# Kernel tuning notes

Hardware: AMD Instinct MI355X
Metric: run time of the kernel (lower is better)

Reference implementation:

```python
import jax, jax.numpy as jnp
import numpy as np
from jax import lax

BETA = 0.3

def setup_inputs() -> dict:
    key = jax.random.key(0)
    ks = jax.random.split(key, 5)
    B, C, H, W = 1, 64, 96, 96
    x = jax.random.normal(ks[0], (B, C, H, W), dtype=jnp.float32)
    # d_conv: Conv2d(C, C, k=3, stride=1, padding=2, dilation=2)
    dW = jax.random.normal(ks[1], (C, C, 3, 3), dtype=jnp.float32) * 0.05
    db = jax.random.normal(ks[2], (C,), dtype=jnp.float32) * 0.05
    # conv: Conv2d(C, C, k=1)
    cW = jax.random.normal(ks[3], (C, C, 1, 1), dtype=jnp.float32) * 0.1
    cb = jax.random.normal(ks[4], (C,), dtype=jnp.float32) * 0.05
    return {"x": x, "dW": dW, "db": db, "cW": cW, "cb": cb}

def _conv(x, w, b, padding, dilation):
    y = lax.conv_general_dilated(
        x, w, window_strides=(1, 1),
        padding=[(padding, padding), (padding, padding)],
        rhs_dilation=(dilation, dilation),
        dimension_numbers=("NCHW", "OIHW", "NCHW"))
    return y + b[None, :, None, None]

def reference(x, dW, db, cW, cb):
    B, C, H, W = x.shape
    HW = H * W
    y = _conv(x, dW, db, padding=2, dilation=2)   # (B,C,H,W), same d_conv used for q and k
    v = _conv(x, cW, cb, padding=0, dilation=1).reshape(B, HW, C)
    # NOTE: torch uses raw .reshape (not transpose) for q — faithful here.
    q = y.reshape(B, HW, C)
    k = y.reshape(B, C, HW)
    qk = jnp.einsum("bnc,bcm->bnm", q, k)         # (B,HW,HW)
    qk = jnp.where(jnp.abs(qk) > BETA, qk, 0.0)   # threshold mask (qk*mask)
    att = jax.nn.softmax(qk, axis=-1)
    att = jnp.einsum("bnm,bmc->bnc", att, v)      # (B,HW,C)
    att = att.swapaxes(1, 2).reshape(B, C, H, W)
    return x + att
```

## Files before the change

kernel.cpp:

```cpp
#include <hip/hip_runtime.h>
#include <hip/hip_bf16.h>

#define CC 64
#define HW 9216
#define IMG 96
#define SPLITS 8
#define SPLEN 1152
#define ITERS 18
#define LOG2E 1.44269504f

typedef _Float16 f16;
typedef __attribute__((ext_vector_type(8))) _Float16 f16x8;
typedef __attribute__((ext_vector_type(4))) _Float16 f16x4;
typedef __attribute__((ext_vector_type(2))) _Float16 f16x2;
typedef __attribute__((ext_vector_type(4))) float f32x4;

__global__ __launch_bounds__(256) void prepad_kernel(
    const float* __restrict__ x, f16* __restrict__ xt)
{
    __shared__ float tile[64][65];
    const int p0 = blockIdx.x * 64;
    const int t = threadIdx.x;
    const int pl = t & 63;
    const int p = p0 + pl;
    int r = p / 100, c = p % 100;
    bool interior = (r >= 2) && (r < 98) && (c >= 2) && (c < 98);
    int img = (r - 2) * IMG + (c - 2);
    #pragma unroll
    for (int j = 0; j < 16; ++j) {
        int ci = j * 4 + (t >> 6);
        tile[pl][ci] = interior ? x[ci * HW + img] : 0.f;
    }
    __syncthreads();
    const int row16 = t >> 4, chunk = t & 15;
    #pragma unroll
    for (int j = 0; j < 4; ++j) {
        int row = j * 16 + row16;
        int pr = p0 + row;
        if (pr < 10000) {
            f16x4 hv = {(f16)tile[row][chunk * 4 + 0], (f16)tile[row][chunk * 4 + 1],
                        (f16)tile[row][chunk * 4 + 2], (f16)tile[row][chunk * 4 + 3]};
            *(f16x4*)&xt[pr * 64 + chunk * 4] = hv;
        }
    }
}

__global__ __launch_bounds__(256) void conv_mfma_kernel(
    const f16* __restrict__ xt, const float* __restrict__ dW, const float* __restrict__ db,
    const float* __restrict__ cW, const float* __restrict__ cb,
    f16* __restrict__ yq, f16* __restrict__ kt, f16* __restrict__ vt)
{
    __shared__ f16 Wl[9 * 16 * 64];
    __shared__ f16 cWl[16 * 64];

    const int b = blockIdx.x;
    const int mblk = b >> 2, cog = b & 3;
    const int co0 = cog * 16;
    const int t = threadIdx.x;

    #pragma unroll 4
    for (int j = 0; j < 36; ++j) {
        int d = j * 256 + t;
        int tap = d >> 10, rem = d & 1023, co = rem >> 6, ci = rem & 63;
        Wl[d] = (f16)dW[(co0 + co) * 576 + ci * 9 + tap];
    }
    #pragma unroll
    for (int j = 0; j < 4; ++j) {
        int d = j * 256 + t;
        cWl[d] = (f16)cW[(co0 + (d >> 6)) * CC + (d & 63)];
    }
    __syncthreads();

    const int w = t >> 6, L = t & 63, g = L >> 4, c16 = L & 15;
    const int ms = mblk * 64 + w * 16;
    const int h = ms / IMG, wc = ms % IMG;
    const int pb = (h + 2) * 100 + (wc + 2) + c16;

    f16x8 Bf[9][2], Bv[2];
    #pragma unroll
    for (int tap = 0; tap < 9; ++tap)
        #pragma unroll
        for (int kc = 0; kc < 2; ++kc)
            Bf[tap][kc] = *(const f16x8*)&Wl[(tap * 16 + c16) * 64 + g * 8 + kc * 32];
    #pragma unroll
    for (int kc = 0; kc < 2; ++kc)
        Bv[kc] = *(const f16x8*)&cWl[c16 * 64 + g * 8 + kc * 32];

    f32x4 accY = (f32x4){0.f, 0.f, 0.f, 0.f};
    f32x4 accV = (f32x4){0.f, 0.f, 0.f, 0.f};

    #pragma unroll
    for (int tap = 0; tap < 9; ++tap) {
        int kh = tap / 3, kw = tap % 3;
        int toff = (2 * kh - 2) * 100 + (2 * kw - 2);
        const f16* ap = xt + (pb + toff) * 64;
        f16x8 A0 = *(const f16x8*)(ap + g * 8);
        f16x8 A1 = *(const f16x8*)(ap + g * 8 + 32);
        accY = __builtin_amdgcn_mfma_f32_16x16x32_f16(A0, Bf[tap][0], accY, 0, 0, 0);
        accY = __builtin_amdgcn_mfma_f32_16x16x32_f16(A1, Bf[tap][1], accY, 0, 0, 0);
        if (tap == 4) {
            accV = __builtin_amdgcn_mfma_f32_16x16x32_f16(A0, Bv[0], accV, 0, 0, 0);
            accV = __builtin_amdgcn_mfma_f32_16x16x32_f16(A1, Bv[1], accV, 0, 0, 0);
        }
    }

    const float dbv = db[co0 + c16], cbv = cb[co0 + c16];
    f16 hy[4];
    #pragma unroll
    for (int j = 0; j < 4; ++j) hy[j] = (f16)(accY[j] + dbv);
    *(f16x4*)&yq[(co0 + c16) * HW + ms + 4 * g] = (f16x4){hy[0], hy[1], hy[2], hy[3]};
    #pragma unroll
    for (int j = 0; j < 4; ++j)
        kt[(ms + 4 * g + j) * 64 + co0 + c16] = hy[j];
    #pragma unroll
    for (int j = 0; j < 4; ++j) {
        int m = ms + 4 * g + j;
        vt[(m & 63) * HW + (co0 + c16) * 144 + (m >> 6)] = (f16)(accV[j] + cbv);
    }
}

__global__ __launch_bounds__(256, 4) void attn_kernel(
    const f16* __restrict__ kt, const f16* __restrict__ vt, const f16* __restrict__ yq,
    f16* __restrict__ acc_ws, float* __restrict__ m_ws, float* __restrict__ l_ws)
{
    __shared__ f16 sKT[64 * 72];
    __shared__ f16 sVT[64 * 72];
    __shared__ f16 sPS[4 * 16 * 72];
    __shared__ float sAL[4 * 16];

    const int t = threadIdx.x;
    const int L = t & 63, w = t >> 6;
    const int g = L >> 4, c16 = L & 15;
    const int qb = blockIdx.x >> 3, sp = blockIdx.x & 7;
    const int n0 = qb * 64;
    const int mbase = sp * SPLEN;
    f16* psw = (f16*)sPS + w * 16 * 72;

    f16x8 qa[2];
    #pragma unroll
    for (int kc = 0; kc < 2; ++kc)
        qa[kc] = *(const f16x8*)(yq + (n0 + w * 16 + c16) * 64 + g * 8 + kc * 32);

    float mi = -1e30f;
    float li = 0.f;
    f32x4 acc[4];
    #pragma unroll
    for (int ct = 0; ct < 4; ++ct) acc[ct] = (f32x4){0.f, 0.f, 0.f, 0.f};

    for (int it = 0; it < ITERS; ++it) {
        const int m0 = mbase + it * 64;
        __syncthreads();
        #pragma unroll
        for (int rep = 0; rep < 2; ++rep) {
            int idx = t + rep * 256;
            int row = idx >> 3, ch = idx & 7;
            *(uint4*)&sKT[row * 72 + ch * 8] = *(const uint4*)&kt[(m0 + row) * 64 + ch * 8];
            *(uint4*)&sVT[row * 72 + ch * 8] = *(const uint4*)&vt[row * HW + m0 + ch * 8];
        }
        __syncthreads();

        f32x4 s[4];
        #pragma unroll
        for (int mt = 0; mt < 4; ++mt) {
            f32x4 a0 = (f32x4){0.f, 0.f, 0.f, 0.f};
            #pragma unroll
            for (int kc = 0; kc < 2; ++kc) {
                f16x8 kb = *(const f16x8*)&sKT[(mt * 16 + c16) * 72 + g * 8 + kc * 32];
                a0 = __builtin_amdgcn_mfma_f32_16x16x32_f16(kb, qa[kc], a0, 0, 0, 0);
            }
            s[mt] = a0;
        }
        #pragma unroll
        for (int mt = 0; mt < 4; ++mt)
            #pragma unroll
            for (int j = 0; j < 4; ++j)
                s[mt][j] = (fabsf(s[mt][j]) > 0.3f) ? s[mt][j] : 0.f;

        float x0 = fmaxf(fmaxf(s[0][0], s[0][1]), fmaxf(s[0][2], s[0][3]));
        float x1 = fmaxf(fmaxf(s[1][0], s[1][1]), fmaxf(s[1][2], s[1][3]));
        float x2 = fmaxf(fmaxf(s[2][0], s[2][1]), fmaxf(s[2][2], s[2][3]));
        float x3 = fmaxf(fmaxf(s[3][0], s[3][1]), fmaxf(s[3][2], s[3][3]));
        float mx = fmaxf(fmaxf(x0, x1), fmaxf(x2, x3));
        mx = fmaxf(mx, __shfl_xor(mx, 16, 64));
        mx = fmaxf(mx, __shfl_xor(mx, 32, 64));
        float mnew = fmaxf(mi, mx);
        float nL = mnew * LOG2E;
        float alpha = __builtin_amdgcn_exp2f(mi * LOG2E - nL);
        mi = mnew;

        float p[16];
        #pragma unroll
        for (int mt = 0; mt < 4; ++mt)
            #pragma unroll
            for (int j = 0; j < 4; ++j)
                p[mt * 4 + j] = __builtin_amdgcn_exp2f(fmaf(s[mt][j], LOG2E, -nL));
        float q0 = (p[0] + p[1]) + (p[2] + p[3]);
        float q1 = (p[4] + p[5]) + (p[6] + p[7]);
        float q2 = (p[8] + p[9]) + (p[10] + p[11]);
        float q3 = (p[12] + p[13]) + (p[14] + p[15]);
        li = li * alpha + ((q0 + q1) + (q2 + q3));

        #pragma unroll
        for (int mt = 0; mt < 4; ++mt) {
            unsigned u0 = __builtin_bit_cast(unsigned int,
                __builtin_amdgcn_cvt_pkrtz(p[mt * 4 + 0], p[mt * 4 + 1]));
            unsigned u1 = __builtin_bit_cast(unsigned int,
                __builtin_amdgcn_cvt_pkrtz(p[mt * 4 + 2], p[mt * 4 + 3]));
            uint2 uv; uv.x = u0; uv.y = u1;
            *(uint2*)&psw[c16 * 72 + mt * 16 + 4 * g] = uv;
        }

        if (g == 0) sAL[w * 16 + c16] = alpha;
        f32x4 aj = *(const f32x4*)&sAL[w * 16 + 4 * g];
        #pragma unroll
        for (int ct = 0; ct < 4; ++ct)
            #pragma unroll
            for (int j = 0; j < 4; ++j) acc[ct][j] *= aj[j];

        f16x8 pa[2];
        #pragma unroll
        for (int kc = 0; kc < 2; ++kc)
            pa[kc] = *(const f16x8*)&psw[c16 * 72 + g * 8 + kc * 32];
        #pragma unroll
        for (int ct = 0; ct < 4; ++ct)
            #pragma unroll
            for (int kc = 0; kc < 2; ++kc) {
                f16x8 vb = *(const f16x8*)&sVT[(ct * 16 + c16) * 72 + g * 8 + kc * 32];
                acc[ct] = __builtin_amdgcn_mfma_f32_16x16x32_f16(pa[kc], vb, acc[ct], 0, 0, 0);
            }
    }

    float li_tot = li;
    li_tot += __shfl_xor(li_tot, 16, 64);
    li_tot += __shfl_xor(li_tot, 32, 64);

    const int base = blockIdx.x;
    #pragma unroll
    for (int ct = 0; ct < 4; ++ct)
        #pragma unroll
        for (int j = 0; j < 4; ++j)
            acc_ws[base * 4096 + (w * 16 + 4 * g + j) * 64 + ct * 16 + c16] = (f16)acc[ct][j];
    if (g == 0) {
        m_ws[base * 64 + w * 16 + c16] = mi;
        l_ws[base * 64 + w * 16 + c16] = li_tot;
    }
}

__global__ __launch_bounds__(256) void merge_kernel(
    const f16* __restrict__ acc_ws, const float* __restrict__ m_ws, const float* __restrict__ l_ws,
    const float* __restrict__ x, float* __restrict__ out)
{
    __shared__ float wsh[SPLITS * 16];
    __shared__ float att[64 * 17];
    const int qb = blockIdx.x >> 2, sub = blockIdx.x & 3;
    const int r0 = sub * 16;
    const int t = threadIdx.x;
    if (t < 16) {
        int row = r0 + t;
        float ms = -1e30f;
        float mv[SPLITS];
        #pragma unroll
        for (int sp = 0; sp < SPLITS; ++sp) {
            mv[sp] = m_ws[(qb * SPLITS + sp) * 64 + row];
            ms = fmaxf(ms, mv[sp]);
        }
        float Lsum = 0.f, ev[SPLITS];
        #pragma unroll
        for (int sp = 0; sp < SPLITS; ++sp) {
            ev[sp] = __builtin_amdgcn_exp2f((mv[sp] - ms) * LOG2E);
            Lsum += l_ws[(qb * SPLITS + sp) * 64 + row] * ev[sp];
        }
        float inv = 1.f / Lsum;
        #pragma unroll
        for (int sp = 0; sp < SPLITS; ++sp)
            wsh[sp * 16 + t] = ev[sp] * inv;
    }
    __syncthreads();
    for (int i = t; i < 1024; i += 256) {
        int rr = i >> 6, c = i & 63;
        float v = 0.f;
        #pragma unroll
        for (int sp = 0; sp < SPLITS; ++sp)
            v += (float)acc_ws[(qb * SPLITS + sp) * 4096 + (r0 + rr) * 64 + c] * wsh[sp * 16 + rr];
        att[c * 17 + rr] = v;
    }
    __syncthreads();
    const int n0 = qb * 64 + r0;
    for (int i = t; i < 1024; i += 256) {
        int c = i >> 4, r = i & 15;
        int idx = c * HW + n0 + r;
        out[idx] = x[idx] + att[c * 17 + r];
    }
}

extern "C" void kernel_launch(void* const* d_in, const int* in_sizes, int n_in,
                              void* d_out, int out_size, void* d_ws, size_t ws_size,
                              hipStream_t stream)
{
    const float* x  = (const float*)d_in[0];
    const float* dW = (const float*)d_in[1];
    const float* db = (const float*)d_in[2];
    const float* cW = (const float*)d_in[3];
    const float* cb = (const float*)d_in[4];
    float* out = (float*)d_out;

    char* ws = (char*)d_ws;
    f16* kt     = (f16*)(ws);
    f16* yq     = (f16*)(ws + 1179648);
    f16* vt     = (f16*)(ws + 2359296);
    f16* xt     = (f16*)(ws + 3538944);
    f16* acc_ws = (f16*)(ws + 4818944);
    float* m_ws = (float*)(ws + 14256128);
    float* l_ws = (float*)(ws + 14551040);

    prepad_kernel<<<dim3(157), dim3(256), 0, stream>>>(x, xt);
    conv_mfma_kernel<<<dim3(576), dim3(256), 0, stream>>>(xt, dW, db, cW, cb, yq, kt, vt);
    attn_kernel<<<dim3(144 * SPLITS), dim3(256), 0, stream>>>(kt, vt, yq, acc_ws, m_ws, l_ws);
    merge_kernel<<<dim3(576), dim3(256), 0, stream>>>(acc_ws, m_ws, l_ws, x, out);
}
```

Before: 141.7 us.

## Switch attention to 32x32x16 MFMA with 128-query blocks per workgroup

The flash-attention kernel now uses 32x32x16 f16 MFMA tiles instead of 16x16x32, and each wave handles 32 query rows, so a block covers 128 queries. The grid is halved and each K/V tile loaded into LDS is reused across twice as many queries, which cuts LDS and global traffic per unit of math and removes one shuffle from the row-max reduction. The workspace layout and the merge kernel indexing change to match. In exchange, register pressure rises (launch bounds drop to 3 blocks per CU) and there are fewer blocks, 576 instead of 1152.

```diff
diff --git a/kernel.cpp b/kernel.cpp
--- a/kernel.cpp
+++ b/kernel.cpp
@@ -12,8 +12,8 @@
 typedef _Float16 f16;
 typedef __attribute__((ext_vector_type(8))) _Float16 f16x8;
 typedef __attribute__((ext_vector_type(4))) _Float16 f16x4;
-typedef __attribute__((ext_vector_type(2))) _Float16 f16x2;
 typedef __attribute__((ext_vector_type(4))) float f32x4;
+typedef __attribute__((ext_vector_type(16))) float f32x16;
 
 __global__ __launch_bounds__(256) void prepad_kernel(
     const float* __restrict__ x, f16* __restrict__ xt)
@@ -119,33 +119,35 @@
     }
 }
 
-__global__ __launch_bounds__(256, 4) void attn_kernel(
+__global__ __launch_bounds__(256, 3) void attn_kernel(
     const f16* __restrict__ kt, const f16* __restrict__ vt, const f16* __restrict__ yq,
     f16* __restrict__ acc_ws, float* __restrict__ m_ws, float* __restrict__ l_ws)
 {
     __shared__ f16 sKT[64 * 72];
     __shared__ f16 sVT[64 * 72];
-    __shared__ f16 sPS[4 * 16 * 72];
-    __shared__ float sAL[4 * 16];
+    __shared__ f16 sPS[4 * 32 * 72];
+    __shared__ float sAL[4 * 32];
 
     const int t = threadIdx.x;
     const int L = t & 63, w = t >> 6;
-    const int g = L >> 4, c16 = L & 15;
+    const int l5 = L >> 5, l31 = L & 31;
     const int qb = blockIdx.x >> 3, sp = blockIdx.x & 7;
-    const int n0 = qb * 64;
+    const int n0 = qb * 128;
     const int mbase = sp * SPLEN;
-    f16* psw = (f16*)sPS + w * 16 * 72;
-
-    f16x8 qa[2];
-    #pragma unroll
-    for (int kc = 0; kc < 2; ++kc)
-        qa[kc] = *(const f16x8*)(yq + (n0 + w * 16 + c16) * 64 + g * 8 + kc * 32);
-
-    float mi = -1e30f;
-    float li = 0.f;
-    f32x4 acc[4];
-    #pragma unroll
-    for (int ct = 0; ct < 4; ++ct) acc[ct] = (f32x4){0.f, 0.f, 0.f, 0.f};
+    f16* psw = (f16*)sPS + w * 32 * 72;
+    float* alw = (float*)sAL + w * 32;
+
+    f16x8 qf[4];
+    #pragma unroll
+    for (int kc = 0; kc < 4; ++kc)
+        qf[kc] = *(const f16x8*)(yq + (n0 + w * 32 + l31) * 64 + kc * 16 + l5 * 8);
+
+    float mi = -1e30f, li = 0.f;
+    f32x16 acc[2];
+    #pragma unroll
+    for (int ct = 0; ct < 2; ++ct)
+        #pragma unroll
+        for (int r = 0; r < 16; ++r) acc[ct][r] = 0.f;
 
     for (int it = 0; it < ITERS; ++it) {
         const int m0 = mbase + it * 64;
@@ -159,90 +161,95 @@
         }
         __syncthreads();
 
-        f32x4 s[4];
-        #pragma unroll
-        for (int mt = 0; mt < 4; ++mt) {
-            f32x4 a0 = (f32x4){0.f, 0.f, 0.f, 0.f};
-            #pragma unroll
-            for (int kc = 0; kc < 2; ++kc) {
-                f16x8 kb = *(const f16x8*)&sKT[(mt * 16 + c16) * 72 + g * 8 + kc * 32];
-                a0 = __builtin_amdgcn_mfma_f32_16x16x32_f16(kb, qa[kc], a0, 0, 0, 0);
+        f32x16 st[2];
+        #pragma unroll
+        for (int kt2 = 0; kt2 < 2; ++kt2) {
+            f32x16 d;
+            #pragma unroll
+            for (int r = 0; r < 16; ++r) d[r] = 0.f;
+            #pragma unroll
+            for (int kc = 0; kc < 4; ++kc) {
+                f16x8 af = *(const f16x8*)&sKT[(kt2 * 32 + l31) * 72 + kc * 16 + l5 * 8];
+                d = __builtin_amdgcn_mfma_f32_32x32x16_f16(af, qf[kc], d, 0, 0, 0);
             }
-            s[mt] = a0;
-        }
-        #pragma unroll
-        for (int mt = 0; mt < 4; ++mt)
-            #pragma unroll
-            for (int j = 0; j < 4; ++j)
-                s[mt][j] = (fabsf(s[mt][j]) > 0.3f) ? s[mt][j] : 0.f;
-
-        float x0 = fmaxf(fmaxf(s[0][0], s[0][1]), fmaxf(s[0][2], s[0][3]));
-        float x1 = fmaxf(fmaxf(s[1][0], s[1][1]), fmaxf(s[1][2], s[1][3]));
-        float x2 = fmaxf(fmaxf(s[2][0], s[2][1]), fmaxf(s[2][2], s[2][3]));
-        float x3 = fmaxf(fmaxf(s[3][0], s[3][1]), fmaxf(s[3][2], s[3][3]));
-        float mx = fmaxf(fmaxf(x0, x1), fmaxf(x2, x3));
-        mx = fmaxf(mx, __shfl_xor(mx, 16, 64));
+            st[kt2] = d;
+        }
+        #pragma unroll
+        for (int kt2 = 0; kt2 < 2; ++kt2)
+            #pragma unroll
+            for (int r = 0; r < 16; ++r)
+                st[kt2][r] = (fabsf(st[kt2][r]) > 0.3f) ? st[kt2][r] : 0.f;
+
+        float q8[8];
+        #pragma unroll
+        for (int kt2 = 0; kt2 < 2; ++kt2)
+            #pragma unroll
+            for (int rq = 0; rq < 4; ++rq)
+                q8[kt2 * 4 + rq] = fmaxf(fmaxf(st[kt2][rq * 4 + 0], st[kt2][rq * 4 + 1]),
+                                         fmaxf(st[kt2][rq * 4 + 2], st[kt2][rq * 4 + 3]));
+        float mx = fmaxf(fmaxf(fmaxf(q8[0], q8[1]), fmaxf(q8[2], q8[3])),
+                         fmaxf(fmaxf(q8[4], q8[5]), fmaxf(q8[6], q8[7])));
         mx = fmaxf(mx, __shfl_xor(mx, 32, 64));
         float mnew = fmaxf(mi, mx);
         float nL = mnew * LOG2E;
         float alpha = __builtin_amdgcn_exp2f(mi * LOG2E - nL);
         mi = mnew;
 
-        float p[16];
-        #pragma unroll
-        for (int mt = 0; mt < 4; ++mt)
-            #pragma unroll
-            for (int j = 0; j < 4; ++j)
-                p[mt * 4 + j] = __builtin_amdgcn_exp2f(fmaf(s[mt][j], LOG2E, -nL));
-        float q0 = (p[0] + p[1]) + (p[2] + p[3]);
-        float q1 = (p[4] + p[5]) + (p[6] + p[7]);
-        float q2 = (p[8] + p[9]) + (p[10] + p[11]);
-        float q3 = (p[12] + p[13]) + (p[14] + p[15]);
-        li = li * alpha + ((q0 + q1) + (q2 + q3));
-
-        #pragma unroll
-        for (int mt = 0; mt < 4; ++mt) {
-            unsigned u0 = __builtin_bit_cast(unsigned int,
-                __builtin_amdgcn_cvt_pkrtz(p[mt * 4 + 0], p[mt * 4 + 1]));
-            unsigned u1 = __builtin_bit_cast(unsigned int,
-                __builtin_amdgcn_cvt_pkrtz(p[mt * 4 + 2], p[mt * 4 + 3]));
-            uint2 uv; uv.x = u0; uv.y = u1;
-            *(uint2*)&psw[c16 * 72 + mt * 16 + 4 * g] = uv;
-        }
-
-        if (g == 0) sAL[w * 16 + c16] = alpha;
-        f32x4 aj = *(const f32x4*)&sAL[w * 16 + 4 * g];
-        #pragma unroll
-        for (int ct = 0; ct < 4; ++ct)
-            #pragma unroll
-            for (int j = 0; j < 4; ++j) acc[ct][j] *= aj[j];
-
-        f16x8 pa[2];
-        #pragma unroll
-        for (int kc = 0; kc < 2; ++kc)
-            pa[kc] = *(const f16x8*)&psw[c16 * 72 + g * 8 + kc * 32];
-        #pragma unroll
-        for (int ct = 0; ct < 4; ++ct)
-            #pragma unroll
-            for (int kc = 0; kc < 2; ++kc) {
-                f16x8 vb = *(const f16x8*)&sVT[(ct * 16 + c16) * 72 + g * 8 + kc * 32];
-                acc[ct] = __builtin_amdgcn_mfma_f32_16x16x32_f16(pa[kc], vb, acc[ct], 0, 0, 0);
+        float ls = 0.f;
+        #pragma unroll
+        for (int kt2 = 0; kt2 < 2; ++kt2)
+            #pragma unroll
+            for (int rq = 0; rq < 4; ++rq) {
+                float p0 = __builtin_amdgcn_exp2f(fmaf(st[kt2][rq * 4 + 0], LOG2E, -nL));
+                float p1 = __builtin_amdgcn_exp2f(fmaf(st[kt2][rq * 4 + 1], LOG2E, -nL));
+                float p2 = __builtin_amdgcn_exp2f(fmaf(st[kt2][rq * 4 + 2], LOG2E, -nL));
+                float p3 = __builtin_amdgcn_exp2f(fmaf(st[kt2][rq * 4 + 3], LOG2E, -nL));
+                ls += (p0 + p1) + (p2 + p3);
+                unsigned u0 = __builtin_bit_cast(unsigned int, __builtin_amdgcn_cvt_pkrtz(p0, p1));
+                unsigned u1 = __builtin_bit_cast(unsigned int, __builtin_amdgcn_cvt_pkrtz(p2, p3));
+                uint2 uv; uv.x = u0; uv.y = u1;
+                *(uint2*)&psw[l31 * 72 + kt2 * 32 + rq * 8 + l5 * 4] = uv;
             }
-    }
-
-    float li_tot = li;
-    li_tot += __shfl_xor(li_tot, 16, 64);
-    li_tot += __shfl_xor(li_tot, 32, 64);
+        li = li * alpha + ls;
+
+        if (l5 == 0) alw[l31] = alpha;
+        f32x4 aj[4];
+        #pragma unroll
+        for (int rq = 0; rq < 4; ++rq)
+            aj[rq] = *(const f32x4*)&alw[rq * 8 + l5 * 4];
+        #pragma unroll
+        for (int ct = 0; ct < 2; ++ct)
+            #pragma unroll
+            for (int r = 0; r < 16; ++r)
+                acc[ct][r] *= aj[r >> 2][r & 3];
+
+        f16x8 pa[4];
+        #pragma unroll
+        for (int kc = 0; kc < 4; ++kc)
+            pa[kc] = *(const f16x8*)&psw[l31 * 72 + kc * 16 + l5 * 8];
+        #pragma unroll
+        for (int ct = 0; ct < 2; ++ct)
+            #pragma unroll
+            for (int kc = 0; kc < 4; ++kc) {
+                f16x8 vb = *(const f16x8*)&sVT[(ct * 32 + l31) * 72 + kc * 16 + l5 * 8];
+                acc[ct] = __builtin_amdgcn_mfma_f32_32x32x16_f16(pa[kc], vb, acc[ct], 0, 0, 0);
+            }
+    }
+
+    float li_tot = li + __shfl_xor(li, 32, 64);
 
     const int base = blockIdx.x;
     #pragma unroll
-    for (int ct = 0; ct < 4; ++ct)
-        #pragma unroll
-        for (int j = 0; j < 4; ++j)
-            acc_ws[base * 4096 + (w * 16 + 4 * g + j) * 64 + ct * 16 + c16] = (f16)acc[ct][j];
-    if (g == 0) {
-        m_ws[base * 64 + w * 16 + c16] = mi;
-        l_ws[base * 64 + w * 16 + c16] = li_tot;
+    for (int ct = 0; ct < 2; ++ct)
+        #pragma unroll
+        for (int r = 0; r < 16; ++r) {
+            int ql = w * 32 + (r & 3) + 8 * (r >> 2) + 4 * l5;
+            int c  = ct * 32 + l31;
+            acc_ws[base * 8192 + ql * 64 + c] = (f16)acc[ct][r];
+        }
+    if (l5 == 0) {
+        m_ws[base * 128 + w * 32 + l31] = mi;
+        l_ws[base * 128 + w * 32 + l31] = li_tot;
     }
 }
 
@@ -252,23 +259,25 @@
 {
     __shared__ float wsh[SPLITS * 16];
     __shared__ float att[64 * 17];
-    const int qb = blockIdx.x >> 2, sub = blockIdx.x & 3;
-    const int r0 = sub * 16;
+    const int b = blockIdx.x;
+    const int row0 = b * 16;
+    const int qb = row0 >> 7;
+    const int ql0 = row0 & 127;
     const int t = threadIdx.x;
     if (t < 16) {
-        int row = r0 + t;
+        int ql = ql0 + t;
         float ms = -1e30f;
         float mv[SPLITS];
         #pragma unroll
         for (int sp = 0; sp < SPLITS; ++sp) {
-            mv[sp] = m_ws[(qb * SPLITS + sp) * 64 + row];
+            mv[sp] = m_ws[(qb * SPLITS + sp) * 128 + ql];
             ms = fmaxf(ms, mv[sp]);
         }
         float Lsum = 0.f, ev[SPLITS];
         #pragma unroll
         for (int sp = 0; sp < SPLITS; ++sp) {
             ev[sp] = __builtin_amdgcn_exp2f((mv[sp] - ms) * LOG2E);
-            Lsum += l_ws[(qb * SPLITS + sp) * 64 + row] * ev[sp];
+            Lsum += l_ws[(qb * SPLITS + sp) * 128 + ql] * ev[sp];
         }
         float inv = 1.f / Lsum;
         #pragma unroll
@@ -281,14 +290,13 @@
         float v = 0.f;
         #pragma unroll
         for (int sp = 0; sp < SPLITS; ++sp)
-            v += (float)acc_ws[(qb * SPLITS + sp) * 4096 + (r0 + rr) * 64 + c] * wsh[sp * 16 + rr];
+            v += (float)acc_ws[(qb * SPLITS + sp) * 8192 + (ql0 + rr) * 64 + c] * wsh[sp * 16 + rr];
         att[c * 17 + rr] = v;
     }
     __syncthreads();
-    const int n0 = qb * 64 + r0;
     for (int i = t; i < 1024; i += 256) {
         int c = i >> 4, r = i & 15;
-        int idx = c * HW + n0 + r;
+        int idx = c * HW + row0 + r;
         out[idx] = x[idx] + att[c * 17 + r];
     }
 }
@@ -315,6 +323,6 @@
 
     prepad_kernel<<<dim3(157), dim3(256), 0, stream>>>(x, xt);
     conv_mfma_kernel<<<dim3(576), dim3(256), 0, stream>>>(xt, dW, db, cW, cb, yq, kt, vt);
-    attn_kernel<<<dim3(144 * SPLITS), dim3(256), 0, stream>>>(kt, vt, yq, acc_ws, m_ws, l_ws);
+    attn_kernel<<<dim3(72 * SPLITS), dim3(256), 0, stream>>>(kt, vt, yq, acc_ws, m_ws, l_ws);
     merge_kernel<<<dim3(576), dim3(256), 0, stream>>>(acc_ws, m_ws, l_ws, x, out);
 }
```

New measurement: 139.6 us. No clear change (-1.5%).
